# Kernel tuning notes

Measured on AMD Instinct MI355X. Metric: run time of the kernel, lower is better.

Reference implementation:

```python
import jax, jax.numpy as jnp
import numpy as np

DIM = 2048; HK = 16; HV = 32; DK = 128; DV = 128; KCONV = 4
EPS = 1e-6; CHUNK = 64
KEY_DIM = HK * DK            # 2048
VALUE_DIM = HV * DV          # 4096
CONV_DIM = 2 * KEY_DIM + VALUE_DIM  # 8192
VR = HV // HK                # 2


def _l2norm(x, eps=1e-6):
    return x * jax.lax.rsqrt(jnp.sum(x * x, -1, keepdims=True) + eps)


def _chunk_gated_delta_rule(q, k, v, g, beta, chunk=CHUNK):
    # q,k: [B,T,H,DK]; v: [B,T,H,DV]; g,beta: [B,T,H]
    B, T, H, Dk = q.shape
    Dv = v.shape[-1]
    N = T // chunk
    q = _l2norm(q) * (Dk ** -0.5)
    k = _l2norm(k)
    rc = lambda t: t.transpose(0, 2, 1, 3).reshape(B, H, N, chunk, t.shape[-1])
    q, k, v = rc(q), rc(k), rc(v)
    g = g.transpose(0, 2, 1).reshape(B, H, N, chunk)
    beta = beta.transpose(0, 2, 1).reshape(B, H, N, chunk)
    v_b = v * beta[..., None]
    k_b = k * beta[..., None]
    g = jnp.cumsum(g, axis=-1)  # intra-chunk cumulative log-decay
    tri = jnp.tril(jnp.ones((chunk, chunk), bool))
    tri_s = jnp.tril(jnp.ones((chunk, chunk), bool), -1)
    diff = g[..., :, None] - g[..., None, :]
    decay = jnp.where(tri, jnp.exp(jnp.where(tri, diff, 0.0)), 0.0)
    # WY representation: T = (I + strict_tril(diag(beta) K K^T decay))^{-1}
    M = jnp.where(tri_s, jnp.einsum('bhnci,bhndi->bhncd', k_b, k) * decay, 0.0)
    eye = jnp.eye(chunk, dtype=q.dtype)
    Tinv = jax.scipy.linalg.solve_triangular(eye + M, jnp.broadcast_to(eye, M.shape), lower=True)
    u = Tinv @ v_b                                  # [B,H,N,C,Dv]
    w = Tinv @ (k_b * jnp.exp(g)[..., None])        # [B,H,N,C,Dk]
    attn_loc = jnp.where(tri, jnp.einsum('bhnci,bhndi->bhncd', q, k) * decay, 0.0)
    qg = q * jnp.exp(g)[..., None]
    g_last = g[..., -1]                             # [B,H,N]
    kdecay = k * jnp.exp(g_last[..., None] - g)[..., None]

    def step(S, inp):  # S: [B,H,Dk,Dv]
        u_i, w_i, a_i, qg_i, kd_i, gl_i = inp
        v_new = u_i - w_i @ S
        o_i = qg_i @ S + a_i @ v_new
        S = S * jnp.exp(gl_i)[..., None, None] + jnp.einsum('bhck,bhcv->bhkv', kd_i, v_new)
        return S, o_i

    S0 = jnp.zeros((B, H, Dk, Dv), q.dtype)
    xs = tuple(jnp.moveaxis(t, 2, 0) for t in (u, w, attn_loc, qg, kdecay, g_last))
    _, o = jax.lax.scan(step, S0, xs)               # [N,B,H,C,Dv]
    return jnp.moveaxis(o, 0, 2).reshape(B, H, T, Dv).transpose(0, 2, 1, 3)


def _forward(x, W_qkvz, W_ba, conv_w, dt_bias, A_log, norm_w, W_out):
    B, T, _ = x.shape
    qkvz = (x @ W_qkvz).reshape(B, T, HK, 2 * DK + 2 * VR * DV)
    ba = (x @ W_ba).reshape(B, T, HK, 2 * VR)
    q, k, v_pre, z_pre = jnp.split(qkvz, [DK, 2 * DK, 2 * DK + VR * DV], axis=3)
    b, a = jnp.split(ba, [VR], axis=3)
    b = b.reshape(B, T, HV)
    a = a.reshape(B, T, HV)
    # mirrors torch: cat -> transpose(1,2) -> reshape(bs,-1,seqlen) (C-order)
    mixed = jnp.concatenate([q, k, v_pre], axis=-1)          # [B,T,HK,512]
    mixed = jnp.transpose(mixed, (0, 2, 1, 3)).reshape(B, -1, T)
    y = jax.lax.conv_general_dilated(
        mixed, conv_w[:, None, :], (1,), [(KCONV - 1, 0)],
        dimension_numbers=('NCH', 'OIH', 'NCH'), feature_group_count=CONV_DIM)
    y = jax.nn.silu(y).transpose(0, 2, 1)                    # [B,T,CONV_DIM]
    q, k, v = jnp.split(y, [KEY_DIM, 2 * KEY_DIM], axis=-1)
    q = q.reshape(B, T, -1, DK)
    k = k.reshape(B, T, -1, DK)
    v = v.reshape(B, T, -1, DV)
    z = z_pre.reshape(B, T, -1, DV)
    beta = jax.nn.sigmoid(b)
    g = -jnp.exp(A_log) * jax.nn.softplus(a + dt_bias)       # [B,T,HV]
    q = jnp.repeat(q, VR, axis=2)
    k = jnp.repeat(k, VR, axis=2)
    o = _chunk_gated_delta_rule(q, k, v, g, beta)            # [B,T,HV,DV]
    # FusedRMSNormGated: gate (silu) before RMS norm
    og = o * jax.nn.silu(z)
    og = og * jax.lax.rsqrt(jnp.mean(og * og, -1, keepdims=True) + EPS) * norm_w
    return og.reshape(B, T, -1) @ W_out


def setup_inputs() -> dict:
    key = jax.random.key(0)
    ks = jax.random.split(key, 8)
    B, T = 1, 4096
    x = jax.random.normal(ks[0], (B, T, DIM), jnp.float32)
    rope_cache = jax.random.normal(ks[1], (T, DK), jnp.float32)
    position_ids = jnp.broadcast_to(jnp.arange(T, dtype=jnp.int32)[None, :], (B, T))
    W_qkvz = jax.random.normal(ks[2], (DIM, 2 * KEY_DIM + 2 * VALUE_DIM), jnp.float32) * (DIM ** -0.5)
    W_ba = jax.random.normal(ks[3], (DIM, 2 * HV), jnp.float32) * (DIM ** -0.5)
    conv_w = jax.random.normal(ks[4], (CONV_DIM, KCONV), jnp.float32) * 0.3
    dt_bias = jnp.ones((HV,), jnp.float32)
    A_log = jnp.log(jax.random.uniform(ks[5], (HV,), jnp.float32, 0.05, 4.0))
    norm_w = jnp.ones((DV,), jnp.float32)
    W_out = jax.random.normal(ks[6], (VALUE_DIM, DIM), jnp.float32) * (VALUE_DIM ** -0.5)
    return {"x": x, "rope_cache": rope_cache, "position_ids": position_ids,
            "W_qkvz": W_qkvz, "W_ba": W_ba, "conv_w": conv_w, "dt_bias": dt_bias,
            "A_log": A_log, "norm_w": norm_w, "W_out": W_out}


def reference(x, rope_cache, position_ids, W_qkvz, W_ba, conv_w, dt_bias, A_log, norm_w, W_out):
    # rope_cache / position_ids are accepted but unused, as in the torch module.
    return _forward(x, W_qkvz, W_ba, conv_w, dt_bias, A_log, norm_w, W_out)
```

## Files before the change

### kernel.cpp

```cpp
#include <hip/hip_runtime.h>
#include <hip/hip_bf16.h>

#define NH_K 16
#define NH_V 32
#define D_K 128
#define D_V 128
#define QKVZ_COLS 12288

typedef __attribute__((ext_vector_type(8))) __bf16 bf16x8;
typedef __attribute__((ext_vector_type(4))) __bf16 bf16x4;
typedef __attribute__((ext_vector_type(4))) float floatx4;
typedef __attribute__((ext_vector_type(4))) unsigned int uint32x4;

#define GLDS16(gp, lp) __builtin_amdgcn_global_load_lds( \
    (const __attribute__((address_space(1))) unsigned int*)(gp), \
    (__attribute__((address_space(3))) unsigned int*)(lp), 16, 0, 0)

__device__ __forceinline__ float sigm(float x) {
  float e = expf(-fabsf(x));
  return (x >= 0.f) ? 1.f / (1.f + e) : e / (1.f + e);
}
__device__ __forceinline__ float clampf(float v, float m) {
  return fminf(fmaxf(v, -m), m);
}
__device__ __forceinline__ float loadF(const void* p, size_t i, bool f32) {
  return f32 ? ((const float*)p)[i] : (float)((const __bf16*)p)[i];
}

__global__ __launch_bounds__(256) void detect_kernel(
    const unsigned int* __restrict__ x, int* __restrict__ flag)
{
  __shared__ int cnt;
  if (threadIdx.x == 0) cnt = 0;
  __syncthreads();
  unsigned int w = x[threadIdx.x];
  int e = (w >> 7) & 0xFF;
  if (e >= 100 && e <= 135) atomicAdd(&cnt, 1);
  __syncthreads();
  if (threadIdx.x == 0) *flag = (cnt < 128) ? 1 : 0;
}

__global__ __launch_bounds__(256) void convx_kernel(
    const void* __restrict__ x, __bf16* __restrict__ xb,
    const int* __restrict__ flagp)
{
  const bool f32 = (*flagp != 0);
  size_t i = ((size_t)blockIdx.x * 256 + threadIdx.x) * 8;
  if (f32) {
    float4 a = *(const float4*)&((const float*)x)[i];
    float4 b = *(const float4*)&((const float*)x)[i + 4];
    bf16x8 v;
    v[0]=(__bf16)a.x; v[1]=(__bf16)a.y; v[2]=(__bf16)a.z; v[3]=(__bf16)a.w;
    v[4]=(__bf16)b.x; v[5]=(__bf16)b.y; v[6]=(__bf16)b.z; v[7]=(__bf16)b.w;
    *(bf16x8*)&xb[i] = v;
  } else {
    *(uint32x4*)&xb[i] = *(const uint32x4*)&((const __bf16*)x)[i];
  }
}

__global__ __launch_bounds__(256) void trans_kernel(
    const void* __restrict__ W, __bf16* __restrict__ WT,
    int K, int N, const int* __restrict__ flagp)
{
  const bool f32 = (*flagp != 0);
  __shared__ float t[32][33];
  const int k0 = blockIdx.x * 32, n0 = blockIdx.y * 32;
  const int tid = threadIdx.x;
  {
    int r = tid >> 3, c4 = (tid & 7) * 4;
    if (f32) {
      float4 v = *(const float4*)&((const float*)W)[(size_t)(k0 + r) * N + n0 + c4];
      t[r][c4] = v.x; t[r][c4 + 1] = v.y; t[r][c4 + 2] = v.z; t[r][c4 + 3] = v.w;
    } else {
      bf16x4 v = *(const bf16x4*)&((const __bf16*)W)[(size_t)(k0 + r) * N + n0 + c4];
      t[r][c4] = (float)v[0]; t[r][c4 + 1] = (float)v[1];
      t[r][c4 + 2] = (float)v[2]; t[r][c4 + 3] = (float)v[3];
    }
  }
  __syncthreads();
  {
    int n = tid >> 3, k4 = (tid & 7) * 4;
    bf16x4 o;
#pragma unroll
    for (int j = 0; j < 4; ++j) o[j] = (__bf16)t[k4 + j][n];
    *(bf16x4*)&WT[(size_t)(n0 + n) * K + k0 + k4] = o;
  }
}

template<bool OUT_F32>
__global__ __launch_bounds__(256) void gemm_bt(
    const __bf16* __restrict__ A, const __bf16* __restrict__ BT,
    void* __restrict__ C, int M, int N, int K)
{
  __shared__ __align__(16) __bf16 As[128 * 32];
  __shared__ __align__(16) __bf16 Bs[128 * 32];
  const int tid = threadIdx.x;
  const int nx  = gridDim.x;
  const int nwg = nx * gridDim.y;
  int lid = blockIdx.y * nx + blockIdx.x;
  int swz = (lid & 7) * (nwg >> 3) + (lid >> 3);
  const int bn = (swz % nx) * 128;
  const int bm = (swz / nx) * 128;
  const int lane = tid & 63;
  const int wv   = tid >> 6;
  const int wm   = (wv >> 1) * 64;
  const int wn   = (wv & 1) * 64;
  const int l15  = lane & 15;
  const int quad = lane >> 4;

  const int o0 = wv * 2048 + lane * 16;
  const int o1 = o0 + 1024;
  const __bf16* Ag0 = &A[(size_t)(bm + (o0 >> 6)) * K + ((o0 & 63) >> 1)];
  const __bf16* Ag1 = &A[(size_t)(bm + (o1 >> 6)) * K + ((o1 & 63) >> 1)];
  const __bf16* Bg0 = &BT[(size_t)(bn + (o0 >> 6)) * K + ((o0 & 63) >> 1)];
  const __bf16* Bg1 = &BT[(size_t)(bn + (o1 >> 6)) * K + ((o1 & 63) >> 1)];
  __bf16* Ad0 = &As[wv * 1024];
  __bf16* Ad1 = &As[wv * 1024 + 512];
  __bf16* Bd0 = &Bs[wv * 1024];
  __bf16* Bd1 = &Bs[wv * 1024 + 512];

  floatx4 acc[4][4];
#pragma unroll
  for (int a = 0; a < 4; ++a)
#pragma unroll
    for (int b = 0; b < 4; ++b)
      acc[a][b] = (floatx4){0.f, 0.f, 0.f, 0.f};

  for (int k0 = 0; k0 < K; k0 += 32) {
    GLDS16(Ag0 + k0, Ad0);
    GLDS16(Ag1 + k0, Ad1);
    GLDS16(Bg0 + k0, Bd0);
    GLDS16(Bg1 + k0, Bd1);
    __syncthreads();
    bf16x8 af[4], bfr[4];
#pragma unroll
    for (int mt = 0; mt < 4; ++mt)
      af[mt] = *(const bf16x8*)&As[(wm + mt * 16 + l15) * 32 + quad * 8];
#pragma unroll
    for (int nt = 0; nt < 4; ++nt)
      bfr[nt] = *(const bf16x8*)&Bs[(wn + nt * 16 + l15) * 32 + quad * 8];
#pragma unroll
    for (int mt = 0; mt < 4; ++mt)
#pragma unroll
      for (int nt = 0; nt < 4; ++nt)
        acc[mt][nt] = __builtin_amdgcn_mfma_f32_16x16x32_bf16(af[mt], bfr[nt], acc[mt][nt], 0, 0, 0);
    __syncthreads();
  }
#pragma unroll
  for (int mt = 0; mt < 4; ++mt)
#pragma unroll
    for (int nt = 0; nt < 4; ++nt)
#pragma unroll
      for (int r = 0; r < 4; ++r) {
        int row = bm + wm + mt * 16 + quad * 4 + r;
        int col = bn + wn + nt * 16 + l15;
        if (OUT_F32) ((float*)C)[(size_t)row * N + col] = acc[mt][nt][r];
        else         ((__bf16*)C)[(size_t)row * N + col] = (__bf16)acc[mt][nt][r];
      }
}

__global__ __launch_bounds__(64) void ba_kernel(
    const void* __restrict__ x, const void* __restrict__ Wba,
    float* __restrict__ ba, const int* __restrict__ flagp)
{
  __shared__ float xr[2048];
  const bool f32 = (*flagp != 0);
  int t = blockIdx.x, tid = threadIdx.x;
  for (int i = tid; i < 2048; i += 64) xr[i] = loadF(x, (size_t)t * 2048 + i, f32);
  __syncthreads();
  float acc = 0.f;
  for (int k = 0; k < 2048; ++k) acc += xr[k] * loadF(Wba, (size_t)k * 64 + tid, f32);
  ba[(size_t)t * 64 + tid] = acc;
}

__global__ __launch_bounds__(256) void conv_kernel(
    const __bf16* __restrict__ qkvz, const void* __restrict__ conv_w,
    __bf16* __restrict__ qn, __bf16* __restrict__ kn, __bf16* __restrict__ vv,
    const int* __restrict__ flagp)
{
  __shared__ __bf16 yin[128][266];
  const bool f32 = (*flagp != 0);
  const int slot = blockIdx.x;
  const int tb   = blockIdx.y;
  const int tid  = threadIdx.x;
  int kind, h_out, cbase;
  if (slot < 16)      { kind = 0; h_out = slot;      cbase = slot * 128; }
  else if (slot < 32) { kind = 1; h_out = slot - 16; cbase = 2048 + h_out * 128; }
  else                { kind = 2; h_out = slot - 32; cbase = 4096 + h_out * 128; }
  const int hc  = cbase >> 9;
  const int cl0 = cbase & 511;
  const int t0  = tb * 256;

  for (int ch = tid; ch < 128 * 33; ch += 256) {
    int d = ch / 33, k = ch - d * 33;
    int s2 = t0 - 8 + k * 8;
    uint32x4 val;
    if (s2 < 0) {
      val = (uint32x4){0u, 0u, 0u, 0u};
    } else {
      int p  = (cl0 + d) * 4096 + s2;
      int tp = p >> 9, ep = p & 511;
      val = *(const uint32x4*)&qkvz[(size_t)tp * QKVZ_COLS + hc * 768 + ep];
    }
    unsigned int* dst = (unsigned int*)&yin[d][k * 8];
    dst[0] = val[0]; dst[1] = val[1]; dst[2] = val[2]; dst[3] = val[3];
  }
  __syncthreads();

  const int wv   = tid >> 6;
  const int lane = tid & 63;
  float w0[4], w1[4];
#pragma unroll
  for (int j = 0; j < 4; ++j) {
    w0[j] = loadF(conv_w, (size_t)(cbase + lane) * 4 + j, f32);
    w1[j] = loadF(conv_w, (size_t)(cbase + lane + 64) * 4 + j, f32);
  }
  const int ltend = wv * 64 + 64;
  for (int lt = wv * 64; lt < ltend; ++lt) {
    int t = t0 + lt;
    float a0 = 0.f, a1 = 0.f;
#pragma unroll
    for (int j = 0; j < 4; ++j) {
      a0 += w0[j] * (float)yin[lane][lt + 5 + j];
      a1 += w1[j] * (float)yin[lane + 64][lt + 5 + j];
    }
    float v0 = a0 * sigm(a0), v1 = a1 * sigm(a1);
    if (kind == 2) {
      vv[((size_t)t * NH_V + h_out) * D_V + lane]      = (__bf16)v0;
      vv[((size_t)t * NH_V + h_out) * D_V + lane + 64] = (__bf16)v1;
    } else {
      float ss = v0 * v0 + v1 * v1;
#pragma unroll
      for (int off = 32; off; off >>= 1) ss += __shfl_xor(ss, off, 64);
      float scl = rsqrtf(ss + 1e-6f);
      if (kind == 0) scl *= 0.08838834764831845f;
      __bf16* dst = (kind == 0) ? qn : kn;
      dst[((size_t)t * NH_K + h_out) * D_K + lane]      = (__bf16)(v0 * scl);
      dst[((size_t)t * NH_K + h_out) * D_K + lane + 64] = (__bf16)(v1 * scl);
    }
  }
}

__global__ __launch_bounds__(64) void gb_kernel(
    const float* __restrict__ ba, const void* __restrict__ dt_bias,
    const void* __restrict__ A_log, float* __restrict__ gbuf,
    float* __restrict__ betabuf, const int* __restrict__ flagp)
{
  const bool f32 = (*flagp != 0);
  int t = blockIdx.x;
  int hv = threadIdx.x;
  if (hv >= 32) return;
  float bv = ba[t * 64 + (hv >> 1) * 4 + (hv & 1)];
  float av = ba[t * 64 + (hv >> 1) * 4 + 2 + (hv & 1)];
  float beta = sigm(bv);
  float xx = av + loadF(dt_bias, hv, f32);
  float sp = (xx > 15.f) ? xx : log1pf(expf(fminf(xx, 15.f)));
  float g = -expf(loadF(A_log, hv, f32)) * sp;
  gbuf[t * 32 + hv] = g;
  betabuf[t * 32 + hv] = beta;
}

__global__ __launch_bounds__(256) void prep_kernel(
    const __bf16* __restrict__ qn, const __bf16* __restrict__ kn, const __bf16* __restrict__ vv,
    const float* __restrict__ gbuf, const float* __restrict__ betabuf,
    float* __restrict__ gcs, __bf16* __restrict__ u, __bf16* __restrict__ w,
    __bf16* __restrict__ attn)
{
  __shared__ float MT[64][67];
  __shared__ __bf16 vT[128][72];
  __shared__ __bf16 kT[128][72];
  __shared__ float gc[64], betas[64], scu[64], scw[64];
  const int bid = blockIdx.x;
  const int hv = bid >> 6, n = bid & 63;
  const int hk = hv >> 1;
  const int t0 = n * 64;
  const int tid = threadIdx.x;
  const int wv = tid >> 6, lane = tid & 63;
  const int l15 = lane & 15, quad = lane >> 4;

  {
    const __bf16* vrow = &vv[((size_t)(t0 + lane) * NH_V + hv) * D_V + wv * 32];
    const __bf16* krow = &kn[((size_t)(t0 + lane) * NH_K + hk) * D_K + wv * 32];
#pragma unroll
    for (int c2 = 0; c2 < 4; ++c2) {
      bf16x8 v8 = *(const bf16x8*)&vrow[c2 * 8];
      bf16x8 k8 = *(const bf16x8*)&krow[c2 * 8];
#pragma unroll
      for (int j = 0; j < 8; ++j) {
        vT[wv * 32 + c2 * 8 + j][lane] = v8[j];
        kT[wv * 32 + c2 * 8 + j][lane] = k8[j];
      }
    }
  }
  if (tid < 64) {
    gc[tid]    = gbuf[(t0 + tid) * 32 + hv];
    betas[tid] = betabuf[(t0 + tid) * 32 + hv];
  }
  __syncthreads();
  if (tid == 0) {
    float s = 0.f;
    for (int i = 0; i < 64; ++i) { s += gc[i]; gc[i] = s; }
  }
  __syncthreads();
  if (tid < 64) {
    float g = gc[tid];
    gcs[((size_t)hv * 64 + n) * 64 + tid] = g;
    scu[tid] = betas[tid];
    scw[tid] = betas[tid] * expf(g);
  }

  floatx4 kk[4];
#pragma unroll
  for (int nt = 0; nt < 4; ++nt) kk[nt] = (floatx4){0.f, 0.f, 0.f, 0.f};
#pragma unroll
  for (int ks = 0; ks < 4; ++ks) {
    bf16x8 afr = *(const bf16x8*)&kn[((size_t)(t0 + wv * 16 + l15) * NH_K + hk) * D_K + ks * 32 + quad * 8];
#pragma unroll
    for (int nt = 0; nt < 4; ++nt) {
      bf16x8 bfr = *(const bf16x8*)&kn[((size_t)(t0 + nt * 16 + l15) * NH_K + hk) * D_K + ks * 32 + quad * 8];
      kk[nt] = __builtin_amdgcn_mfma_f32_16x16x32_bf16(afr, bfr, kk[nt], 0, 0, 0);
    }
  }
#pragma unroll
  for (int nt = 0; nt < 4; ++nt)
#pragma unroll
    for (int r = 0; r < 4; ++r) {
      int i = wv * 16 + quad * 4 + r;
      int j = nt * 16 + l15;
      float m = 0.f;
      if (j < i) m = kk[nt][r] * betas[i] * expf(fminf(gc[i] - gc[j], 0.f));
      MT[i][j] = m;
    }
  __syncthreads();

  if (wv == 0) {
    if (lane == 0) MT[0][0] = 1.f;
    for (int ii = 1; ii < 64; ++ii) {
      float s = 0.f;
      for (int l = 0; l < ii; ++l) s += MT[ii][l] * MT[l][lane];
      MT[ii][lane] = ((lane == ii) ? 1.f : 0.f) - s;
    }
  }
  {
    int band = (wv == 0) ? 3 : (wv - 1);
    floatx4 at[4];
#pragma unroll
    for (int nt = 0; nt < 4; ++nt) at[nt] = (floatx4){0.f, 0.f, 0.f, 0.f};
#pragma unroll
    for (int ks = 0; ks < 4; ++ks) {
      bf16x8 afr = *(const bf16x8*)&qn[((size_t)(t0 + band * 16 + l15) * NH_K + hk) * D_K + ks * 32 + quad * 8];
#pragma unroll
      for (int nt = 0; nt < 4; ++nt) {
        bf16x8 bfr = *(const bf16x8*)&kn[((size_t)(t0 + nt * 16 + l15) * NH_K + hk) * D_K + ks * 32 + quad * 8];
        at[nt] = __builtin_amdgcn_mfma_f32_16x16x32_bf16(afr, bfr, at[nt], 0, 0, 0);
      }
    }
    size_t abase = ((size_t)hv * 64 + n) * (64 * 64);
#pragma unroll
    for (int nt = 0; nt < 4; ++nt)
#pragma unroll
      for (int r = 0; r < 4; ++r) {
        int i = band * 16 + quad * 4 + r;
        int j = nt * 16 + l15;
        float dec = expf(fminf(gc[i] - gc[j], 0.f));
        float a = (j <= i) ? clampf(at[nt][r] * dec, 1e6f) : 0.f;
        attn[abase + (size_t)i * 64 + j] = (__bf16)a;
      }
  }
  __syncthreads();

  floatx4 ua[8], wa[8];
#pragma unroll
  for (int t = 0; t < 8; ++t) {
    ua[t] = (floatx4){0.f, 0.f, 0.f, 0.f};
    wa[t] = (floatx4){0.f, 0.f, 0.f, 0.f};
  }
#pragma unroll
  for (int ks = 0; ks < 2; ++ks) {
    bf16x8 uh, ul, wh, wl;
#pragma unroll
    for (int j = 0; j < 8; ++j) {
      int c = ks * 32 + quad * 8 + j;
      float raw = MT[wv * 16 + l15][c];
      float tu = raw * scu[c];
      float tw = raw * scw[c];
      __bf16 h1 = (__bf16)tu; uh[j] = h1; ul[j] = (__bf16)(tu - (float)h1);
      __bf16 h2 = (__bf16)tw; wh[j] = h2; wl[j] = (__bf16)(tw - (float)h2);
    }
#pragma unroll
    for (int nt = 0; nt < 8; ++nt) {
      bf16x8 vb = *(const bf16x8*)&vT[nt * 16 + l15][ks * 32 + quad * 8];
      ua[nt] = __builtin_amdgcn_mfma_f32_16x16x32_bf16(uh, vb, ua[nt], 0, 0, 0);
      ua[nt] = __builtin_amdgcn_mfma_f32_16x16x32_bf16(ul, vb, ua[nt], 0, 0, 0);
      bf16x8 kb = *(const bf16x8*)&kT[nt * 16 + l15][ks * 32 + quad * 8];
      wa[nt] = __builtin_amdgcn_mfma_f32_16x16x32_bf16(wh, kb, wa[nt], 0, 0, 0);
      wa[nt] = __builtin_amdgcn_mfma_f32_16x16x32_bf16(wl, kb, wa[nt], 0, 0, 0);
    }
  }
  size_t base = ((size_t)hv * 64 + n) * (64 * 128);
#pragma unroll
  for (int nt = 0; nt < 8; ++nt)
#pragma unroll
    for (int r = 0; r < 4; ++r) {
      int row = wv * 16 + quad * 4 + r;
      int dv  = nt * 16 + l15;
      u[base + (size_t)row * 128 + dv] = (__bf16)clampf(ua[nt][r], 1e6f);
      w[base + (size_t)row * 128 + dv] = (__bf16)clampf(wa[nt][r], 1e6f);
    }
}

__global__ __launch_bounds__(64, 1) void scan_kernel(
    const __bf16* __restrict__ u, const __bf16* __restrict__ w, const __bf16* __restrict__ attn,
    const __bf16* __restrict__ qn, const __bf16* __restrict__ kn, const float* __restrict__ gcs,
    __bf16* __restrict__ obuf)
{
  __shared__ __bf16 sb_hi[16][136];
  __shared__ __bf16 sb_lo[16][136];
  __shared__ __bf16 vt[16][72];
  __shared__ __bf16 kt[128][72];

  const int hv   = blockIdx.x & 31;
  const int band = blockIdx.x >> 5;
  const int dv0  = band * 16;
  const int hk   = hv >> 1;
  const int lane = threadIdx.x;
  const int l15  = lane & 15;
  const int quad = lane >> 4;

  floatx4 S[8];
#pragma unroll
  for (int m = 0; m < 8; ++m) S[m] = (floatx4){0.f, 0.f, 0.f, 0.f};
  for (int i = lane; i < 16 * 136 / 2; i += 64) {
    ((unsigned int*)sb_hi)[i] = 0u;
    ((unsigned int*)sb_lo)[i] = 0u;
  }

  for (int n = 0; n < 64; ++n) {
    const int t0 = n * 64;
    const size_t cb = (size_t)hv * 64 + n;
    const float* gr = gcs + cb * 64;
    const size_t ub = cb * 8192;

    const __bf16* krow = &kn[((size_t)(t0 + lane) * NH_K + hk) * D_K];
    bf16x8 kr[16];
#pragma unroll
    for (int c2 = 0; c2 < 16; ++c2) kr[c2] = *(const bf16x8*)&krow[c2 * 8];

    floatx4 av[4];
#pragma unroll
    for (int mt = 0; mt < 4; ++mt)
#pragma unroll
      for (int r = 0; r < 4; ++r)
        av[mt][r] = (float)u[ub + (size_t)(mt * 16 + quad * 4 + r) * 128 + dv0 + l15];

    bf16x8 sh[4], sl[4];
#pragma unroll
    for (int ks = 0; ks < 4; ++ks) {
      sh[ks] = *(const bf16x8*)&sb_hi[l15][ks * 32 + quad * 8];
      sl[ks] = *(const bf16x8*)&sb_lo[l15][ks * 32 + quad * 8];
    }

#pragma unroll
    for (int ks = 0; ks < 4; ++ks)
#pragma unroll
      for (int mt = 0; mt < 4; ++mt) {
        uint32x4 wu = *(const uint32x4*)&w[ub + (size_t)(mt * 16 + l15) * 128 + ks * 32 + quad * 8];
        wu[0] ^= 0x80008000u; wu[1] ^= 0x80008000u;
        wu[2] ^= 0x80008000u; wu[3] ^= 0x80008000u;
        bf16x8 wf = __builtin_bit_cast(bf16x8, wu);
        av[mt] = __builtin_amdgcn_mfma_f32_16x16x32_bf16(wf, sh[ks], av[mt], 0, 0, 0);
        av[mt] = __builtin_amdgcn_mfma_f32_16x16x32_bf16(wf, sl[ks], av[mt], 0, 0, 0);
      }
#pragma unroll
    for (int mt = 0; mt < 4; ++mt) {
      bf16x4 h4;
#pragma unroll
      for (int r = 0; r < 4; ++r) h4[r] = (__bf16)clampf(av[mt][r], 1e8f);
      *(bf16x4*)&vt[l15][mt * 16 + quad * 4] = h4;
    }

    const float gl  = gr[63];
    const float egl = expf(gl);
    float egr[16];
#pragma unroll
    for (int mt = 0; mt < 4; ++mt)
#pragma unroll
      for (int r = 0; r < 4; ++r)
        egr[mt * 4 + r] = expf(gr[mt * 16 + quad * 4 + r]);
    float ek0[8], ek1[8];
#pragma unroll
    for (int j = 0; j < 8; ++j) {
      ek0[j] = expf(fminf(gl - gr[quad * 8 + j], 0.f));
      ek1[j] = expf(fminf(gl - gr[32 + quad * 8 + j], 0.f));
    }

    floatx4 ao[4];
#pragma unroll
    for (int mt = 0; mt < 4; ++mt) ao[mt] = (floatx4){0.f, 0.f, 0.f, 0.f};
#pragma unroll
    for (int ks = 0; ks < 4; ++ks)
#pragma unroll
      for (int mt = 0; mt < 4; ++mt) {
        bf16x8 qf = *(const bf16x8*)&qn[((size_t)(t0 + mt * 16 + l15) * NH_K + hk) * D_K + ks * 32 + quad * 8];
        ao[mt] = __builtin_amdgcn_mfma_f32_16x16x32_bf16(qf, sh[ks], ao[mt], 0, 0, 0);
        ao[mt] = __builtin_amdgcn_mfma_f32_16x16x32_bf16(qf, sl[ks], ao[mt], 0, 0, 0);
      }
#pragma unroll
    for (int mt = 0; mt < 4; ++mt)
#pragma unroll
      for (int r = 0; r < 4; ++r) ao[mt][r] *= egr[mt * 4 + r];

#pragma unroll
    for (int c2 = 0; c2 < 16; ++c2)
#pragma unroll
      for (int j = 0; j < 8; ++j)
        kt[c2 * 8 + j][lane] = kr[c2][j];

    bf16x8 vf0 = *(const bf16x8*)&vt[l15][quad * 8];
    bf16x8 vf1 = *(const bf16x8*)&vt[l15][32 + quad * 8];
#pragma unroll
    for (int mt = 0; mt < 4; ++mt) {
      bf16x8 a0 = *(const bf16x8*)&attn[cb * 4096 + (size_t)(mt * 16 + l15) * 64 + quad * 8];
      bf16x8 a1 = *(const bf16x8*)&attn[cb * 4096 + (size_t)(mt * 16 + l15) * 64 + 32 + quad * 8];
      ao[mt] = __builtin_amdgcn_mfma_f32_16x16x32_bf16(a0, vf0, ao[mt], 0, 0, 0);
      ao[mt] = __builtin_amdgcn_mfma_f32_16x16x32_bf16(a1, vf1, ao[mt], 0, 0, 0);
    }
#pragma unroll
    for (int mt = 0; mt < 4; ++mt)
#pragma unroll
      for (int r = 0; r < 4; ++r)
        obuf[((size_t)(t0 + mt * 16 + quad * 4 + r) * NH_V + hv) * D_V + dv0 + l15]
            = (__bf16)clampf(ao[mt][r], 1e8f);

#pragma unroll
    for (int m = 0; m < 8; ++m)
#pragma unroll
      for (int r = 0; r < 4; ++r) S[m][r] *= egl;
    bf16x8 vfd0, vfd1;
#pragma unroll
    for (int j = 0; j < 8; ++j) {
      vfd0[j] = (__bf16)((float)vf0[j] * ek0[j]);
      vfd1[j] = (__bf16)((float)vf1[j] * ek1[j]);
    }
#pragma unroll
    for (int ks = 0; ks < 2; ++ks) {
      bf16x8 vf = ks ? vfd1 : vfd0;
#pragma unroll
      for (int m = 0; m < 8; ++m) {
        bf16x8 kf = *(const bf16x8*)&kt[m * 16 + l15][ks * 32 + quad * 8];
        S[m] = __builtin_amdgcn_mfma_f32_16x16x32_bf16(kf, vf, S[m], 0, 0, 0);
      }
    }
#pragma unroll
    for (int m = 0; m < 8; ++m) {
      bf16x4 h4, l4;
#pragma unroll
      for (int r = 0; r < 4; ++r) {
        float v = clampf(S[m][r], 1e8f);
        S[m][r] = v;
        __bf16 h = (__bf16)v;
        h4[r] = h;
        l4[r] = (__bf16)(v - (float)h);
      }
      *(bf16x4*)&sb_hi[l15][m * 16 + quad * 4] = h4;
      *(bf16x4*)&sb_lo[l15][m * 16 + quad * 4] = l4;
    }
  }
}

__global__ __launch_bounds__(128) void gate_kernel(
    const __bf16* __restrict__ obuf, const __bf16* __restrict__ qkvz,
    const void* __restrict__ norm_w, __bf16* __restrict__ og,
    const int* __restrict__ flagp)
{
  const bool f32 = (*flagp != 0);
  int t = blockIdx.x, hv = blockIdx.y, d = threadIdx.x;
  float ov = (float)obuf[((size_t)t * NH_V + hv) * D_V + d];
  float z = (float)qkvz[(size_t)t * QKVZ_COLS + (hv >> 1) * 768 + 512 + (hv & 1) * 128 + d];
  float val = ov * (z * sigm(z));
  __shared__ float red[128];
  red[d] = val * val;
  __syncthreads();
  for (int s = 64; s >= 1; s >>= 1) {
    if (d < s) red[d] += red[d + s];
    __syncthreads();
  }
  float scl = rsqrtf(red[0] * (1.f / 128.f) + 1e-6f);
  og[(size_t)t * 4096 + hv * 128 + d] = (__bf16)(val * scl * loadF(norm_w, d, f32));
}

extern "C" void kernel_launch(void* const* d_in, const int* in_sizes, int n_in,
                              void* d_out, int out_size, void* d_ws, size_t ws_size,
                              hipStream_t stream) {
  (void)in_sizes; (void)n_in; (void)out_size;
  const void* x     = d_in[0];
  const void* Wqkvz = d_in[3];
  const void* Wba   = d_in[4];
  const void* convw = d_in[5];
  const void* dtb   = d_in[6];
  const void* Alog  = d_in[7];
  const void* normw = d_in[8];
  const void* Wout  = d_in[9];

  char* ws = (char*)d_ws;
  size_t off = 0;
  int*    flag = (int*)(ws + off);    off += 256;
  __bf16* qkvz = (__bf16*)(ws + off); off += (size_t)4096 * 12288 * 2;
  float* ba    = (float*)(ws + off);  off += (size_t)4096 * 64 * 4;
  float* gbuf  = (float*)(ws + off);  off += (size_t)4096 * 32 * 4;
  float* betab = (float*)(ws + off);  off += (size_t)4096 * 32 * 4;
  float* gcs   = (float*)(ws + off);  off += (size_t)32 * 64 * 64 * 4;
  __bf16* qn   = (__bf16*)(ws + off); off += (size_t)4096 * 2048 * 2;
  __bf16* kn   = (__bf16*)(ws + off); off += (size_t)4096 * 2048 * 2;
  __bf16* vv   = (__bf16*)(ws + off); off += (size_t)4096 * 4096 * 2;
  __bf16* ubuf = (__bf16*)(ws + off); off += (size_t)32 * 64 * 8192 * 2;
  __bf16* wbuf = (__bf16*)(ws + off); off += (size_t)32 * 64 * 8192 * 2;
  __bf16* attn = (__bf16*)(ws + off); off += (size_t)32 * 64 * 4096 * 2;
  __bf16* obuf = vv;
  __bf16* og   = ubuf;
  __bf16* WqkvzT = ubuf;
  __bf16* xb     = attn;
  __bf16* WoutT  = wbuf;
  if (ws_size < off) return;

  detect_kernel<<<1, 256, 0, stream>>>((const unsigned int*)x, flag);
  convx_kernel<<<4096, 256, 0, stream>>>(x, xb, flag);
  trans_kernel<<<dim3(64, 384), 256, 0, stream>>>(Wqkvz, WqkvzT, 2048, 12288, flag);
  gemm_bt<false><<<dim3(96, 32), 256, 0, stream>>>(xb, WqkvzT, qkvz, 4096, 12288, 2048);
  ba_kernel<<<4096, 64, 0, stream>>>(x, Wba, ba, flag);
  conv_kernel<<<dim3(64, 16), 256, 0, stream>>>(qkvz, convw, qn, kn, vv, flag);
  gb_kernel<<<4096, 64, 0, stream>>>(ba, dtb, Alog, gbuf, betab, flag);
  prep_kernel<<<2048, 256, 0, stream>>>(qn, kn, vv, gbuf, betab, gcs, ubuf, wbuf, attn);
  scan_kernel<<<256, 64, 0, stream>>>(ubuf, wbuf, attn, qn, kn, gcs, obuf);
  gate_kernel<<<dim3(4096, 32), 128, 0, stream>>>(obuf, qkvz, normw, og, flag);
  trans_kernel<<<dim3(128, 64), 256, 0, stream>>>(Wout, WoutT, 4096, 2048, flag);
  gemm_bt<true><<<dim3(16, 32), 256, 0, stream>>>(og, WoutT, d_out, 4096, 2048, 4096);
}
```

Baseline: 1.461 ms.

## Use 256x256 double-buffered swizzled GEMM and warp-shuffle gate normalization

Replaces the 128x128 single-buffered MFMA GEMM with a 512-thread 256x256 tile kernel that double-buffers LDS via global_load_lds, applies an XOR swizzle to avoid bank conflicts, and overlaps the next tile's loads with compute using explicit waitcnt. Separately, the gating RMSNorm kernel now processes four heads per block with two elements per lane and a wavefront shuffle reduction instead of a shared-memory tree. The larger tile raises data reuse but yields only 128 blocks for the output projection, which may underfill the GPU.

```diff
diff --git a/kernel.cpp b/kernel.cpp
--- a/kernel.cpp
+++ b/kernel.cpp
@@ -9,6 +9,7 @@
 
 typedef __attribute__((ext_vector_type(8))) __bf16 bf16x8;
 typedef __attribute__((ext_vector_type(4))) __bf16 bf16x4;
+typedef __attribute__((ext_vector_type(2))) __bf16 bf16x2;
 typedef __attribute__((ext_vector_type(4))) float floatx4;
 typedef __attribute__((ext_vector_type(4))) unsigned int uint32x4;
 
@@ -88,72 +89,94 @@
 }
 
 template<bool OUT_F32>
-__global__ __launch_bounds__(256) void gemm_bt(
+__global__ __launch_bounds__(512, 1) void gemm_bt2(
     const __bf16* __restrict__ A, const __bf16* __restrict__ BT,
     void* __restrict__ C, int M, int N, int K)
 {
-  __shared__ __align__(16) __bf16 As[128 * 32];
-  __shared__ __align__(16) __bf16 Bs[128 * 32];
+  __shared__ __align__(16) __bf16 As[2][8192];
+  __shared__ __align__(16) __bf16 Bs[2][8192];
   const int tid = threadIdx.x;
   const int nx  = gridDim.x;
   const int nwg = nx * gridDim.y;
   int lid = blockIdx.y * nx + blockIdx.x;
   int swz = (lid & 7) * (nwg >> 3) + (lid >> 3);
-  const int bn = (swz % nx) * 128;
-  const int bm = (swz / nx) * 128;
+  const int bn = (swz % nx) * 256;
+  const int bm = (swz / nx) * 256;
   const int lane = tid & 63;
   const int wv   = tid >> 6;
-  const int wm   = (wv >> 1) * 64;
-  const int wn   = (wv & 1) * 64;
+  const int wm2  = wv >> 2;
+  const int wn2  = wv & 3;
   const int l15  = lane & 15;
   const int quad = lane >> 4;
-
-  const int o0 = wv * 2048 + lane * 16;
-  const int o1 = o0 + 1024;
-  const __bf16* Ag0 = &A[(size_t)(bm + (o0 >> 6)) * K + ((o0 & 63) >> 1)];
-  const __bf16* Ag1 = &A[(size_t)(bm + (o1 >> 6)) * K + ((o1 & 63) >> 1)];
-  const __bf16* Bg0 = &BT[(size_t)(bn + (o0 >> 6)) * K + ((o0 & 63) >> 1)];
-  const __bf16* Bg1 = &BT[(size_t)(bn + (o1 >> 6)) * K + ((o1 & 63) >> 1)];
-  __bf16* Ad0 = &As[wv * 1024];
-  __bf16* Ad1 = &As[wv * 1024 + 512];
-  __bf16* Bd0 = &Bs[wv * 1024];
-  __bf16* Bd1 = &Bs[wv * 1024 + 512];
-
-  floatx4 acc[4][4];
-#pragma unroll
-  for (int a = 0; a < 4; ++a)
+  const int NT   = K >> 5;
+
+  auto stage = [&](int kt, int slot) {
+    const int k0 = kt * 32;
+#pragma unroll
+    for (int L = 0; L < 2; ++L) {
+      const int boff = L * 8192 + wv * 1024 + lane * 16;
+      const int swb  = boff ^ (((boff >> 9) & 1) << 5);
+      const int row  = swb >> 6;
+      const int ce   = (swb & 63) >> 1;
+      GLDS16(&A[(size_t)(bm + row) * K + k0 + ce], &As[slot][L * 4096 + wv * 512]);
+      GLDS16(&BT[(size_t)(bn + row) * K + k0 + ce], &Bs[slot][L * 4096 + wv * 512]);
+    }
+  };
+
+  floatx4 acc[8][4];
+#pragma unroll
+  for (int a = 0; a < 8; ++a)
 #pragma unroll
     for (int b = 0; b < 4; ++b)
       acc[a][b] = (floatx4){0.f, 0.f, 0.f, 0.f};
 
-  for (int k0 = 0; k0 < K; k0 += 32) {
-    GLDS16(Ag0 + k0, Ad0);
-    GLDS16(Ag1 + k0, Ad1);
-    GLDS16(Bg0 + k0, Bd0);
-    GLDS16(Bg1 + k0, Bd1);
-    __syncthreads();
-    bf16x8 af[4], bfr[4];
-#pragma unroll
-    for (int mt = 0; mt < 4; ++mt)
-      af[mt] = *(const bf16x8*)&As[(wm + mt * 16 + l15) * 32 + quad * 8];
+  const int flip  = (l15 & 8) ? 32 : 0;
+  const int baseA = (((wm2 * 128 + l15) * 64 + quad * 16) ^ flip);
+  const int baseB = (((wn2 * 64 + l15) * 64 + quad * 16) ^ flip);
+
+  stage(0, 0);
+  stage(1, 1);
+  asm volatile("s_waitcnt vmcnt(4)" ::: "memory");
+  __builtin_amdgcn_s_barrier();
+  __builtin_amdgcn_sched_barrier(0);
+
+  for (int kt = 0; kt < NT; ++kt) {
+    const int cur = kt & 1;
+    const char* Ab = (const char*)&As[cur][0];
+    const char* Bb = (const char*)&Bs[cur][0];
+    bf16x8 af[8], bfr[4];
+#pragma unroll
+    for (int mt = 0; mt < 8; ++mt)
+      af[mt] = *(const bf16x8*)(Ab + baseA + mt * 1024);
 #pragma unroll
     for (int nt = 0; nt < 4; ++nt)
-      bfr[nt] = *(const bf16x8*)&Bs[(wn + nt * 16 + l15) * 32 + quad * 8];
-#pragma unroll
-    for (int mt = 0; mt < 4; ++mt)
+      bfr[nt] = *(const bf16x8*)(Bb + baseB + nt * 1024);
+#pragma unroll
+    for (int mt = 0; mt < 8; ++mt)
 #pragma unroll
       for (int nt = 0; nt < 4; ++nt)
         acc[mt][nt] = __builtin_amdgcn_mfma_f32_16x16x32_bf16(af[mt], bfr[nt], acc[mt][nt], 0, 0, 0);
-    __syncthreads();
-  }
-#pragma unroll
-  for (int mt = 0; mt < 4; ++mt)
+    if (kt + 1 < NT) {
+      __builtin_amdgcn_s_barrier();
+      if (kt + 2 < NT) {
+        stage(kt + 2, cur);
+        asm volatile("s_waitcnt vmcnt(4)" ::: "memory");
+      } else {
+        asm volatile("s_waitcnt vmcnt(0)" ::: "memory");
+      }
+      __builtin_amdgcn_s_barrier();
+      __builtin_amdgcn_sched_barrier(0);
+    }
+  }
+
+#pragma unroll
+  for (int mt = 0; mt < 8; ++mt)
 #pragma unroll
     for (int nt = 0; nt < 4; ++nt)
 #pragma unroll
       for (int r = 0; r < 4; ++r) {
-        int row = bm + wm + mt * 16 + quad * 4 + r;
-        int col = bn + wn + nt * 16 + l15;
+        int row = bm + wm2 * 128 + mt * 16 + quad * 4 + r;
+        int col = bn + wn2 * 64 + nt * 16 + l15;
         if (OUT_F32) ((float*)C)[(size_t)row * N + col] = acc[mt][nt][r];
         else         ((__bf16*)C)[(size_t)row * N + col] = (__bf16)acc[mt][nt][r];
       }
@@ -568,25 +591,29 @@
   }
 }
 
-__global__ __launch_bounds__(128) void gate_kernel(
+__global__ __launch_bounds__(256) void gate_kernel(
     const __bf16* __restrict__ obuf, const __bf16* __restrict__ qkvz,
     const void* __restrict__ norm_w, __bf16* __restrict__ og,
     const int* __restrict__ flagp)
 {
   const bool f32 = (*flagp != 0);
-  int t = blockIdx.x, hv = blockIdx.y, d = threadIdx.x;
-  float ov = (float)obuf[((size_t)t * NH_V + hv) * D_V + d];
-  float z = (float)qkvz[(size_t)t * QKVZ_COLS + (hv >> 1) * 768 + 512 + (hv & 1) * 128 + d];
-  float val = ov * (z * sigm(z));
-  __shared__ float red[128];
-  red[d] = val * val;
-  __syncthreads();
-  for (int s = 64; s >= 1; s >>= 1) {
-    if (d < s) red[d] += red[d + s];
-    __syncthreads();
-  }
-  float scl = rsqrtf(red[0] * (1.f / 128.f) + 1e-6f);
-  og[(size_t)t * 4096 + hv * 128 + d] = (__bf16)(val * scl * loadF(norm_w, d, f32));
+  const int t = blockIdx.x;
+  const int wv = threadIdx.x >> 6, lane = threadIdx.x & 63;
+  const int hv = blockIdx.y * 4 + wv;
+  const int d = lane * 2;
+  bf16x2 ov = *(const bf16x2*)&obuf[((size_t)t * NH_V + hv) * D_V + d];
+  bf16x2 zv = *(const bf16x2*)&qkvz[(size_t)t * QKVZ_COLS + (hv >> 1) * 768 + 512 + (hv & 1) * 128 + d];
+  float z0 = (float)zv[0], z1 = (float)zv[1];
+  float v0 = (float)ov[0] * (z0 * sigm(z0));
+  float v1 = (float)ov[1] * (z1 * sigm(z1));
+  float ss = v0 * v0 + v1 * v1;
+#pragma unroll
+  for (int off = 32; off; off >>= 1) ss += __shfl_xor(ss, off, 64);
+  float scl = rsqrtf(ss * (1.f / 128.f) + 1e-6f);
+  bf16x2 o;
+  o[0] = (__bf16)(v0 * scl * loadF(norm_w, d, f32));
+  o[1] = (__bf16)(v1 * scl * loadF(norm_w, d + 1, f32));
+  *(bf16x2*)&og[(size_t)t * 4096 + hv * 128 + d] = o;
 }
 
 extern "C" void kernel_launch(void* const* d_in, const int* in_sizes, int n_in,
@@ -626,13 +653,13 @@
   detect_kernel<<<1, 256, 0, stream>>>((const unsigned int*)x, flag);
   convx_kernel<<<4096, 256, 0, stream>>>(x, xb, flag);
   trans_kernel<<<dim3(64, 384), 256, 0, stream>>>(Wqkvz, WqkvzT, 2048, 12288, flag);
-  gemm_bt<false><<<dim3(96, 32), 256, 0, stream>>>(xb, WqkvzT, qkvz, 4096, 12288, 2048);
+  gemm_bt2<false><<<dim3(48, 16), 512, 0, stream>>>(xb, WqkvzT, qkvz, 4096, 12288, 2048);
   ba_kernel<<<4096, 64, 0, stream>>>(x, Wba, ba, flag);
   conv_kernel<<<dim3(64, 16), 256, 0, stream>>>(qkvz, convw, qn, kn, vv, flag);
   gb_kernel<<<4096, 64, 0, stream>>>(ba, dtb, Alog, gbuf, betab, flag);
   prep_kernel<<<2048, 256, 0, stream>>>(qn, kn, vv, gbuf, betab, gcs, ubuf, wbuf, attn);
   scan_kernel<<<256, 64, 0, stream>>>(ubuf, wbuf, attn, qn, kn, gcs, obuf);
-  gate_kernel<<<dim3(4096, 32), 128, 0, stream>>>(obuf, qkvz, normw, og, flag);
+  gate_kernel<<<dim3(4096, 8), 256, 0, stream>>>(obuf, qkvz, normw, og, flag);
   trans_kernel<<<dim3(128, 64), 256, 0, stream>>>(Wout, WoutT, 4096, 2048, flag);
-  gemm_bt<true><<<dim3(16, 32), 256, 0, stream>>>(og, WoutT, d_out, 4096, 2048, 4096);
-}
+  gemm_bt2<true><<<dim3(8, 16), 512, 0, stream>>>(og, WoutT, d_out, 4096, 2048, 4096);
+}
```

After: 1.486 ms. Within noise of the previous version (+1.7%).
